# Kernel optimization log

Hardware: AMD Instinct MI355X
Metric: run time of the kernel (lower is better)

The kernel has to match this reference:

```python
import jax, jax.numpy as jnp
import numpy as np

K_NEIGHBORS = 6
LN_EPS = 1e-5


def _layernorm(h, g, b):
    m = h.mean(-1, keepdims=True)
    v = h.var(-1, keepdims=True)
    return (h - m) / jnp.sqrt(v + LN_EPS) * g + b


def _mlp(h, w0, b0, w1, b1):
    return jax.nn.relu(h @ w0 + b0) @ w1 + b1


def _learn_adj(x, Wp, bp):
    # EfficientGraphStructureLearner: cosine-sim topk graph, symmetrized, row-normalized
    h = x @ Wp + bp
    nrm = jnp.linalg.norm(h, axis=1, keepdims=True)
    h = h / jnp.maximum(nrm, 1e-12)
    S = h @ h.T                                  # [N, N]
    vals, idx = jax.lax.top_k(S, K_NEIGHBORS + 1)  # col 0 is self (diag == 1)
    N = x.shape[0]
    rows = jnp.arange(N)[:, None]
    adj = jnp.zeros_like(S).at[rows, idx[:, 1:]].set(vals[:, 1:])
    adj = (adj + adj.T) * 0.5
    adj = adj / (adj.sum(1, keepdims=True) + 1e-8)
    return adj


def _gcn(h, adj, W, b):
    # StandardGraphConv: D^-1/2 (A+I) D^-1/2 @ (h W) + b (diag matmuls as row/col scaling)
    A = adj + jnp.eye(adj.shape[0], dtype=adj.dtype)
    d = jnp.maximum(A.sum(1), 1e-12) ** -0.5
    norm_adj = d[:, None] * A * d[None, :]
    return norm_adj @ (h @ W) + b


def setup_inputs() -> dict:
    key = jax.random.key(0)
    ks = iter(jax.random.split(key, 40))
    N, D, H, O, HP = 8192, 20, 32, 128, 16
    f = lambda *s: jax.random.normal(next(ks), s, dtype=jnp.float32) * 0.1
    inp = {
        'x': jax.random.normal(next(ks), (N, D), dtype=jnp.float32),
        'Wp': f(D, HP), 'bp': jnp.zeros((HP,), jnp.float32),
        'gw0': f(D, H), 'gb0': jnp.zeros((H,), jnp.float32),
        'gw1': f(H, H), 'gb1': jnp.zeros((H,), jnp.float32),
        'gw2': f(H, O), 'gb2': jnp.zeros((O,), jnp.float32),
        'lg0': jnp.ones((H,), jnp.float32), 'lb0': jnp.zeros((H,), jnp.float32),
        'lg1': jnp.ones((H,), jnp.float32), 'lb1': jnp.zeros((H,), jnp.float32),
        'lg2': jnp.ones((O,), jnp.float32), 'lb2': jnp.zeros((O,), jnp.float32),
        'riw0': f(D, H), 'rib0': jnp.zeros((H,), jnp.float32),
        'riw1': f(H, H), 'rib1': jnp.zeros((H,), jnp.float32),
        'rhw0': f(H, H), 'rhb0': jnp.zeros((H,), jnp.float32),
        'rhw1': f(H, H), 'rhb1': jnp.zeros((H,), jnp.float32),
        'row0': f(H, O), 'rob0': jnp.zeros((O,), jnp.float32),
        'row1': f(O, O), 'rob1': jnp.zeros((O,), jnp.float32),
    }
    return inp


def reference(x, Wp, bp, gw0, gb0, gw1, gb1, gw2, gb2,
              lg0, lb0, lg1, lb1, lg2, lb2,
              riw0, rib0, riw1, rib1,
              rhw0, rhb0, rhw1, rhb1,
              row0, rob0, row1, rob1):
    adj = _learn_adj(x, Wp, bp)
    gcns = [(gw0, gb0, lg0, lb0), (gw1, gb1, lg1, lb1), (gw2, gb2, lg2, lb2)]
    skips = [(riw0, rib0, riw1, rib1), (rhw0, rhb0, rhw1, rhb1), (row0, rob0, row1, rob1)]
    h = x
    for i, ((W, b, g, bt), sk) in enumerate(zip(gcns, skips)):
        h_new = jax.nn.relu(_layernorm(_gcn(h, adj, W, b), g, bt))
        h = h_new + _mlp(h, *sk)
        # dropout is identity in eval mode
    return h
```

## Files before the change

### kernel.cpp

```cpp
#include <hip/hip_runtime.h>

constexpr int D_IN = 20;
constexpr int HP   = 16;
constexpr int K    = 6;
constexpr int SAMP = 512;
constexpr int NC   = 8;
constexpr int CAPC = 192;
constexpr int CIN  = 128;
constexpr float MARGIN = 0.02f;

typedef __attribute__((ext_vector_type(8))) short bf16x8;
typedef __attribute__((ext_vector_type(4))) float f32x4;

__device__ __forceinline__ float dot16_seq(const float4* q, const float4* c) {
  float s = 0.f;
#pragma unroll
  for (int m = 0; m < 4; ++m) {
    s = fmaf(q[m].x, c[m].x, s);
    s = fmaf(q[m].y, c[m].y, s);
    s = fmaf(q[m].z, c[m].z, s);
    s = fmaf(q[m].w, c[m].w, s);
  }
  return s;
}

__device__ __forceinline__ short f2bf(float f) {
  unsigned u = __float_as_uint(f);
  unsigned r = (u + 0x7fffu + ((u >> 16) & 1u)) >> 16;
  return (short)r;
}

__device__ __forceinline__ float dinv_of(float own, float ins) {
  float rs = 0.5f * (own + ins);
  float rn = 1.f / (rs + 1e-8f);
  return rsqrtf(fmaxf(1.f + rs * rn, 1e-12f));
}

__global__ void k_proj(const float* __restrict__ x, const float* __restrict__ Wp,
                       const float* __restrict__ bp, const float* __restrict__ gw0,
                       float* __restrict__ hn, short* __restrict__ hnb,
                       float* __restrict__ XW0,
                       float* __restrict__ insum, int* __restrict__ indeg, int N) {
  int i = blockIdx.x * blockDim.x + threadIdx.x;
  if (i >= N) return;
  insum[i] = 0.f; indeg[i] = 0;
  float xr[D_IN];
#pragma unroll
  for (int d = 0; d < D_IN; ++d) xr[d] = x[i*D_IN + d];
  float hv[HP];
  float nrm2 = 0.f;
#pragma unroll
  for (int h = 0; h < HP; ++h) {
    float a = bp[h];
#pragma unroll
    for (int d = 0; d < D_IN; ++d) a += xr[d] * Wp[d*HP + h];
    hv[h] = a;
    nrm2 += a * a;
  }
  float inv = 1.f / fmaxf(sqrtf(nrm2), 1e-12f);
#pragma unroll
  for (int h = 0; h < HP; ++h) {
    float v = hv[h] * inv;
    hn[i*HP + h] = v;
    hnb[(size_t)i*32 + h] = f2bf(v);
  }
#pragma unroll
  for (int h = 0; h < HP; ++h) hnb[(size_t)i*32 + 16 + h] = 0;
#pragma unroll
  for (int oc = 0; oc < 32; ++oc) {
    float a = 0.f;
#pragma unroll
    for (int d = 0; d < D_IN; ++d) a += xr[d] * gw0[d*32 + oc];
    XW0[(size_t)i*32 + oc] = a;
  }
}

struct Top6 { float v0,v1,v2,v3,v4,v5; int i0,i1,i2,i3,i4,i5; };

__device__ __forceinline__ void t6_init(Top6& t) {
  t.v0=t.v1=t.v2=t.v3=t.v4=t.v5=-1e30f;
  t.i0=t.i1=t.i2=t.i3=t.i4=t.i5=-1;
}

#define T6_SWAP(a,b,ia,ib) { float tv=a; a=b; b=tv; int ti=ia; ia=ib; ib=ti; }

__device__ __forceinline__ void t6_insert(Top6& t, float s, int c) {
  if (s > t.v5) {
    t.v5 = s; t.i5 = c;
    if (t.v5 > t.v4) { T6_SWAP(t.v4, t.v5, t.i4, t.i5); }
    if (t.v4 > t.v3) { T6_SWAP(t.v3, t.v4, t.i3, t.i4); }
    if (t.v3 > t.v2) { T6_SWAP(t.v2, t.v3, t.i2, t.i3); }
    if (t.v2 > t.v1) { T6_SWAP(t.v1, t.v2, t.i1, t.i2); }
    if (t.v1 > t.v0) { T6_SWAP(t.v0, t.v1, t.i0, t.i1); }
  }
}

__device__ __forceinline__ void t6_best(const Top6& t, float& cv, int& ci) {
  cv = t.v0; ci = t.i0;
  if (t.v1 > cv || (t.v1 == cv && (unsigned)t.i1 < (unsigned)ci)) { cv = t.v1; ci = t.i1; }
  if (t.v2 > cv || (t.v2 == cv && (unsigned)t.i2 < (unsigned)ci)) { cv = t.v2; ci = t.i2; }
  if (t.v3 > cv || (t.v3 == cv && (unsigned)t.i3 < (unsigned)ci)) { cv = t.v3; ci = t.i3; }
  if (t.v4 > cv || (t.v4 == cv && (unsigned)t.i4 < (unsigned)ci)) { cv = t.v4; ci = t.i4; }
  if (t.v5 > cv || (t.v5 == cv && (unsigned)t.i5 < (unsigned)ci)) { cv = t.v5; ci = t.i5; }
}

__device__ __forceinline__ void t6_consume(Top6& t, int mi) {
  if (t.i0 == mi) t.v0 = -1e30f;
  if (t.i1 == mi) t.v1 = -1e30f;
  if (t.i2 == mi) t.v2 = -1e30f;
  if (t.i3 == mi) t.v3 = -1e30f;
  if (t.i4 == mi) t.v4 = -1e30f;
  if (t.i5 == mi) t.v5 = -1e30f;
}

__global__ __launch_bounds__(256) void k_thresh(const float* __restrict__ hn,
                                                float* __restrict__ tau, int N) {
  int wave = threadIdx.x >> 6, lane = threadIdx.x & 63;
  int row = blockIdx.x * 4 + wave;
  const float4* hn4 = (const float4*)hn;
  float4 q[4];
#pragma unroll
  for (int m = 0; m < 4; ++m) q[m] = hn4[(size_t)row*4 + m];
  Top6 t; t6_init(t);
#pragma unroll
  for (int k = 0; k < SAMP/64; ++k) {
    int c = lane + 64*k;
    if (c != row) {
      float4 cv[4];
#pragma unroll
      for (int m = 0; m < 4; ++m) cv[m] = hn4[(size_t)c*4 + m];
      float s = dot16_seq(q, cv);
      t6_insert(t, s, c);
    }
  }
  float last = -1e30f;
  for (int sel = 0; sel < K; ++sel) {
    float cv; int ci;
    t6_best(t, cv, ci);
    float mv = cv; int mi = ci;
#pragma unroll
    for (int m = 1; m < 64; m <<= 1) {
      float ov = __shfl_xor(mv, m);
      int   oi = __shfl_xor(mi, m);
      if (ov > mv || (ov == mv && (unsigned)oi < (unsigned)mi)) { mv = ov; mi = oi; }
    }
    t6_consume(t, mi);
    last = mv;
  }
  if (lane == 0) tau[row] = last;
}

__global__ __launch_bounds__(256) void k_scan2(
    const short* __restrict__ hnb, const float* __restrict__ tau,
    int* __restrict__ cnt, unsigned short* __restrict__ buf, int N) {
  __shared__ int cntl[16];
  int rb = blockIdx.x / NC;
  int jc = blockIdx.x % NC;
  int wave = threadIdx.x >> 6, lane = threadIdx.x & 63;
  int r0 = rb * 16;
  int half = lane >> 4;
  int l16  = lane & 15;

  if (threadIdx.x < 16) cntl[threadIdx.x] = 0;
  __syncthreads();

  bf16x8 a = *(const bf16x8*)(hnb + (size_t)(r0 + l16)*32 + half*8);
  float4 t4 = *(const float4*)(tau + r0 + half*4);
  float tm0 = t4.x - MARGIN, tm1 = t4.y - MARGIN,
        tm2 = t4.z - MARGIN, tm3 = t4.w - MARGIN;
  f32x4 zero = {0.f, 0.f, 0.f, 0.f};

  const int SPANW = N / NC / 4;
  int jb0 = jc * (N / NC) + wave * SPANW;

#define APPB(R, COND)                                                        \
  {                                                                          \
    unsigned long long mr = __ballot(COND);                                  \
    if (l16 == 0) {                                                          \
      unsigned mask = (unsigned)(mr >> (16*half)) & 0xFFFFu;                 \
      if (mask) {                                                            \
        int row = r0 + half*4 + (R);                                         \
        int pos = atomicAdd(&cntl[4*half + (R)], __popc(mask));              \
        unsigned mm = mask;                                                  \
        while (mm) {                                                         \
          int bx = __ffs(mm) - 1; mm &= mm - 1;                              \
          if (pos < CAPC)                                                    \
            buf[((size_t)row*NC + jc)*CAPC + pos] = (unsigned short)(jb + bx); \
          ++pos;                                                             \
        }                                                                    \
      }                                                                      \
    }                                                                        \
  }

#pragma unroll 4
  for (int jt = 0; jt < SPANW; jt += 16) {
    int jb = jb0 + jt;
    bf16x8 b = *(const bf16x8*)(hnb + (size_t)(jb + l16)*32 + half*8);
    f32x4 d = __builtin_amdgcn_mfma_f32_16x16x32_bf16(a, b, zero, 0, 0, 0);
    bool h0 = d[0] >= tm0, h1 = d[1] >= tm1, h2 = d[2] >= tm2, h3 = d[3] >= tm3;
    if (__any(h0 | h1 | h2 | h3)) {
      APPB(0, h0) APPB(1, h1) APPB(2, h2) APPB(3, h3)
    }
  }
#undef APPB

  __syncthreads();
  if (threadIdx.x < 16)
    cnt[(size_t)(r0 + threadIdx.x)*NC + jc] = min(cntl[threadIdx.x], CAPC);
}

__global__ __launch_bounds__(256) void k_final(
    const float* __restrict__ hn, const unsigned short* __restrict__ buf,
    const int* __restrict__ cnt,
    float* __restrict__ evals, int* __restrict__ eidx,
    float* __restrict__ ownsum, float* insum, int* indeg,
    unsigned short* __restrict__ incol, float* __restrict__ inval, int N) {
  int wave = threadIdx.x >> 6, lane = threadIdx.x & 63;
  int row = blockIdx.x * 4 + wave;
  const float4* hn4 = (const float4*)hn;
  float4 q[4];
#pragma unroll
  for (int m = 0; m < 4; ++m) q[m] = hn4[(size_t)row*4 + m];

  int cbase = row * NC;
  int cl = (lane < NC) ? cnt[cbase + lane] : 0;
  int c0 = __shfl(cl, 0), c1 = __shfl(cl, 1), c2 = __shfl(cl, 2), c3 = __shfl(cl, 3),
      c4 = __shfl(cl, 4), c5 = __shfl(cl, 5), c6 = __shfl(cl, 6), c7 = __shfl(cl, 7);
  int p1 = c0, p2 = p1 + c1, p3 = p2 + c2, p4 = p3 + c3,
      p5 = p4 + c4, p6 = p5 + c5, p7 = p6 + c6, T = p7 + c7;

  Top6 t; t6_init(t);
  for (int e = lane; e < T; e += 64) {
    int s, off;
    if (e < p4) {
      if (e < p2) { if (e < p1) { s = 0; off = e; } else { s = 1; off = e - p1; } }
      else        { if (e < p3) { s = 2; off = e - p2; } else { s = 3; off = e - p3; } }
    } else {
      if (e < p6) { if (e < p5) { s = 4; off = e - p4; } else { s = 5; off = e - p5; } }
      else        { if (e < p7) { s = 6; off = e - p6; } else { s = 7; off = e - p7; } }
    }
    int j = buf[((size_t)cbase + s)*CAPC + off];
    if (j != row) {
      float4 cv[4];
#pragma unroll
      for (int m = 0; m < 4; ++m) cv[m] = hn4[(size_t)j*4 + m];
      float sc = dot16_seq(q, cv);
      t6_insert(t, sc, j);
    }
  }
  float osum = 0.f;
  for (int sel = 0; sel < K; ++sel) {
    float cv; int ci;
    t6_best(t, cv, ci);
    float mv = cv; int mi = ci;
#pragma unroll
    for (int m = 1; m < 64; m <<= 1) {
      float ov = __shfl_xor(mv, m);
      int   oi = __shfl_xor(mi, m);
      if (ov > mv || (ov == mv && (unsigned)oi < (unsigned)mi)) { mv = ov; mi = oi; }
    }
    t6_consume(t, mi);
    if (lane == 0) {
      evals[row*K + sel] = mv;
      eidx [row*K + sel] = mi;
      osum += mv;
      atomicAdd(&insum[mi], mv);
      int pos = atomicAdd(&indeg[mi], 1);
      if (pos < CIN) {
        incol[(size_t)mi*CIN + pos] = (unsigned short)row;
        inval[(size_t)mi*CIN + pos] = mv;
      }
    }
  }
  if (lane == 0) ownsum[row] = osum;
}

template<int DIN, int NEXTD, bool SCALED>
__global__ __launch_bounds__(256) void k_gpost32(
    const float* __restrict__ XWsrc,
    const int* __restrict__ eidx, const float* __restrict__ evals,
    const unsigned short* __restrict__ incol, const float* __restrict__ inval,
    const int* __restrict__ indeg,
    const float* __restrict__ ownsum, const float* __restrict__ insum,
    const float* __restrict__ gb, const float* __restrict__ lg, const float* __restrict__ lb,
    const float* __restrict__ hprev,
    const float* __restrict__ w0, const float* __restrict__ b0,
    const float* __restrict__ w1, const float* __restrict__ b1,
    const float* __restrict__ Wnext, float* __restrict__ XWnext,
    float* __restrict__ outp, int N) {
  __shared__ float hid[4][2][32];
  int tid = threadIdx.x;
  int lane = tid & 63, wslot = tid >> 6;
  int sub = lane >> 5, ol = lane & 31;
  int row = (blockIdx.x * 4 + wslot) * 2 + sub;

  float rs_i = 0.5f * (ownsum[row] + insum[row]);
  float rn_i = 1.f / (rs_i + 1e-8f);
  float di_i = rsqrtf(fmaxf(1.f + rs_i * rn_i, 1e-12f));
  float cc = 0.5f * di_i * rn_i;
  float acc = (SCALED ? di_i : di_i * di_i) * XWsrc[(size_t)row*32 + ol];
#pragma unroll
  for (int t = 0; t < K; ++t) {
    int j = eidx[row*K + t]; float v = evals[row*K + t];
    float cf;
    if constexpr (SCALED) cf = cc * v;
    else                  cf = cc * v * dinv_of(ownsum[j], insum[j]);
    acc = fmaf(cf, XWsrc[(size_t)j*32 + ol], acc);
  }
  int ne = min(indeg[row], CIN);
  for (int e = 0; e < ne; ++e) {
    int j = incol[(size_t)row*CIN + e]; float v = inval[(size_t)row*CIN + e];
    float cf;
    if constexpr (SCALED) cf = cc * v;
    else                  cf = cc * v * dinv_of(ownsum[j], insum[j]);
    acc = fmaf(cf, XWsrc[(size_t)j*32 + ol], acc);
  }
  float u0 = acc + gb[ol];
  float s = u0;
#pragma unroll
  for (int m = 1; m < 32; m <<= 1) s += __shfl_xor(s, m);
  float mean = s * (1.f/32.f);
  float d0 = u0 - mean;
  float vs = d0*d0;
#pragma unroll
  for (int m = 1; m < 32; m <<= 1) vs += __shfl_xor(vs, m);
  float rstd = rsqrtf(vs * (1.f/32.f) + 1e-5f);
  float t0 = fmaxf(d0*rstd*lg[ol] + lb[ol], 0.f);

  float hp[DIN];
#pragma unroll
  for (int d = 0; d < DIN; ++d) hp[d] = hprev[(size_t)row*DIN + d];
  float a = b0[ol];
#pragma unroll
  for (int d = 0; d < DIN; ++d) a = fmaf(hp[d], w0[d*32 + ol], a);
  hid[wslot][sub][ol] = fmaxf(a, 0.f);
  float o = b1[ol];
#pragma unroll
  for (int h = 0; h < 32; ++h) o = fmaf(hid[wslot][sub][h], w1[h*32 + ol], o);
  float hv = t0 + o;
  outp[(size_t)row*32 + ol] = hv;

  hid[wslot][sub][ol] = hv;
#pragma unroll
  for (int k2 = 0; k2 < NEXTD/32; ++k2) {
    int oc = ol + 32*k2;
    float acc2 = 0.f;
#pragma unroll
    for (int d = 0; d < 32; ++d)
      acc2 = fmaf(hid[wslot][sub][d], Wnext[d*NEXTD + oc], acc2);
    XWnext[(size_t)row*NEXTD + oc] = di_i * acc2;
  }
}

__global__ __launch_bounds__(256) void k_gpost128(
    const float* __restrict__ XW,
    const int* __restrict__ eidx, const float* __restrict__ evals,
    const unsigned short* __restrict__ incol, const float* __restrict__ inval,
    const int* __restrict__ indeg,
    const float* __restrict__ ownsum, const float* __restrict__ insum,
    const float* __restrict__ b, const float* __restrict__ g, const float* __restrict__ bt,
    const float* __restrict__ hprev,
    const float* __restrict__ w0, const float* __restrict__ b0,
    const float* __restrict__ w1, const float* __restrict__ b1,
    float* __restrict__ out, int N) {
  __shared__ float hid_s[4][128];
  __shared__ float w1s[2048];
  int wslot = threadIdx.x >> 6;
  int row   = (blockIdx.x * blockDim.x + threadIdx.x) >> 6;
  int lane  = threadIdx.x & 63;
  int o0 = lane, o1 = lane + 64;

  float rs_i = 0.5f * (ownsum[row] + insum[row]);
  float rn_i = 1.f / (rs_i + 1e-8f);
  float di_i = rsqrtf(fmaxf(1.f + rs_i * rn_i, 1e-12f));
  float cc = 0.5f * di_i * rn_i;
  float acc0 = di_i * XW[(size_t)row*128 + o0];
  float acc1 = di_i * XW[(size_t)row*128 + o1];
#pragma unroll
  for (int t = 0; t < K; ++t) {
    int j = eidx[row*K + t];
    float cf = cc * evals[row*K + t];
    acc0 = fmaf(cf, XW[(size_t)j*128 + o0], acc0);
    acc1 = fmaf(cf, XW[(size_t)j*128 + o1], acc1);
  }
  int ne = min(indeg[row], CIN);
  for (int e = 0; e < ne; ++e) {
    int j = incol[(size_t)row*CIN + e];
    float cf = cc * inval[(size_t)row*CIN + e];
    acc0 = fmaf(cf, XW[(size_t)j*128 + o0], acc0);
    acc1 = fmaf(cf, XW[(size_t)j*128 + o1], acc1);
  }
  float u0 = acc0 + b[o0];
  float u1 = acc1 + b[o1];

  float s = u0 + u1;
#pragma unroll
  for (int m = 1; m < 64; m <<= 1) s += __shfl_xor(s, m);
  float mean = s * (1.f/128.f);
  float d0 = u0 - mean, d1 = u1 - mean;
  float vs = d0*d0 + d1*d1;
#pragma unroll
  for (int m = 1; m < 64; m <<= 1) vs += __shfl_xor(vs, m);
  float rstd = rsqrtf(vs * (1.f/128.f) + 1e-5f);
  float t0 = fmaxf(d0*rstd*g[o0] + bt[o0], 0.f);
  float t1 = fmaxf(d1*rstd*g[o1] + bt[o1], 0.f);

  float hp[32];
#pragma unroll
  for (int d = 0; d < 32; ++d) hp[d] = hprev[(size_t)row*32 + d];
  {
    float a = b0[o0];
#pragma unroll
    for (int d = 0; d < 32; ++d) a = fmaf(hp[d], w0[d*128 + o0], a);
    hid_s[wslot][o0] = fmaxf(a, 0.f);
    float a1 = b0[o1];
#pragma unroll
    for (int d = 0; d < 32; ++d) a1 = fmaf(hp[d], w0[d*128 + o1], a1);
    hid_s[wslot][o1] = fmaxf(a1, 0.f);
  }

  float r0=0.f, r1=0.f, r2=0.f, r3=0.f, q0=0.f, q1=0.f, q2=0.f, q3=0.f;
  for (int c = 0; c < 8; ++c) {
    __syncthreads();
    {
      const float4* src = (const float4*)(w1 + c*2048);
      float4* dst = (float4*)w1s;
      dst[threadIdx.x]       = src[threadIdx.x];
      dst[threadIdx.x + 256] = src[threadIdx.x + 256];
    }
    __syncthreads();
    int hb = c*16;
#pragma unroll
    for (int hh = 0; hh < 16; hh += 4) {
      float h0 = hid_s[wslot][hb+hh+0], h1 = hid_s[wslot][hb+hh+1],
            h2 = hid_s[wslot][hb+hh+2], h3 = hid_s[wslot][hb+hh+3];
      r0 = fmaf(h0, w1s[(hh+0)*128 + o0], r0); q0 = fmaf(h0, w1s[(hh+0)*128 + o1], q0);
      r1 = fmaf(h1, w1s[(hh+1)*128 + o0], r1); q1 = fmaf(h1, w1s[(hh+1)*128 + o1], q1);
      r2 = fmaf(h2, w1s[(hh+2)*128 + o0], r2); q2 = fmaf(h2, w1s[(hh+2)*128 + o1], q2);
      r3 = fmaf(h3, w1s[(hh+3)*128 + o0], r3); q3 = fmaf(h3, w1s[(hh+3)*128 + o1], q3);
    }
  }
  out[(size_t)row*128 + o0] = t0 + b1[o0] + ((r0 + r1) + (r2 + r3));
  out[(size_t)row*128 + o1] = t1 + b1[o1] + ((q0 + q1) + (q2 + q3));
}

extern "C" void kernel_launch(void* const* d_in, const int* in_sizes, int n_in,
                              void* d_out, int out_size, void* d_ws, size_t ws_size,
                              hipStream_t stream) {
  const float* x    = (const float*)d_in[0];
  const float* Wp   = (const float*)d_in[1];
  const float* bp   = (const float*)d_in[2];
  const float* gw0  = (const float*)d_in[3];
  const float* gb0  = (const float*)d_in[4];
  const float* gw1  = (const float*)d_in[5];
  const float* gb1  = (const float*)d_in[6];
  const float* gw2  = (const float*)d_in[7];
  const float* gb2  = (const float*)d_in[8];
  const float* lg0  = (const float*)d_in[9];
  const float* lb0  = (const float*)d_in[10];
  const float* lg1  = (const float*)d_in[11];
  const float* lb1  = (const float*)d_in[12];
  const float* lg2  = (const float*)d_in[13];
  const float* lb2  = (const float*)d_in[14];
  const float* riw0 = (const float*)d_in[15];
  const float* rib0 = (const float*)d_in[16];
  const float* riw1 = (const float*)d_in[17];
  const float* rib1 = (const float*)d_in[18];
  const float* rhw0 = (const float*)d_in[19];
  const float* rhb0 = (const float*)d_in[20];
  const float* rhw1 = (const float*)d_in[21];
  const float* rhb1 = (const float*)d_in[22];
  const float* row0 = (const float*)d_in[23];
  const float* rob0 = (const float*)d_in[24];
  const float* row1 = (const float*)d_in[25];
  const float* rob1 = (const float*)d_in[26];
  int N = in_sizes[0] / D_IN;
  float* out = (float*)d_out;

  char* ws = (char*)d_ws;
  size_t off = 0;
  auto alloc = [&](size_t bytes) -> void* {
    void* p = ws + off;
    off += (bytes + 255) & ~(size_t)255;
    return p;
  };
  float* hn      = (float*)alloc((size_t)N * HP * 4);
  float* evals   = (float*)alloc((size_t)N * K * 4);
  int*   eidx    = (int*)  alloc((size_t)N * K * 4);
  float* ownsum  = (float*)alloc((size_t)N * 4);
  float* insum   = (float*)alloc((size_t)N * 4);
  int*   indeg   = (int*)  alloc((size_t)N * 4);
  float* XWa     = (float*)alloc((size_t)N * 128 * 4);
  float* XWb     = (float*)alloc((size_t)N * 32 * 4);
  float* h1      = (float*)alloc((size_t)N * 32 * 4);
  float* h2      = (float*)alloc((size_t)N * 32 * 4);
  float* tau     = (float*)alloc((size_t)N * 4);
  int*   cnt     = (int*)  alloc((size_t)N * NC * 4);
  unsigned short* buf = (unsigned short*)alloc((size_t)N * NC * CAPC * 2);
  short* hnb     = (short*)alloc((size_t)N * 32 * 2);
  unsigned short* incol = (unsigned short*)alloc((size_t)N * CIN * 2);
  float* inval   = (float*)alloc((size_t)N * CIN * 4);
  (void)ws_size; (void)n_in; (void)out_size;

  const int B = 256;
  hipLaunchKernelGGL(k_proj, dim3((N + B - 1) / B), dim3(B), 0, stream,
                     x, Wp, bp, gw0, hn, hnb, XWa, insum, indeg, N);
  hipLaunchKernelGGL(k_thresh, dim3(N / 4), dim3(B), 0, stream, hn, tau, N);
  hipLaunchKernelGGL(k_scan2, dim3((N / 16) * NC), dim3(B), 0, stream, hnb, tau, cnt, buf, N);
  hipLaunchKernelGGL(k_final, dim3(N / 4), dim3(B), 0, stream,
                     hn, buf, cnt, evals, eidx, ownsum, insum, indeg, incol, inval, N);

  hipLaunchKernelGGL((k_gpost32<20, 32, false>), dim3(N / 8), dim3(B), 0, stream,
                     XWa, eidx, evals, incol, inval, indeg, ownsum, insum,
                     gb0, lg0, lb0, x, riw0, rib0, riw1, rib1, gw1, XWb, h1, N);
  hipLaunchKernelGGL((k_gpost32<32, 128, true>), dim3(N / 8), dim3(B), 0, stream,
                     XWb, eidx, evals, incol, inval, indeg, ownsum, insum,
                     gb1, lg1, lb1, h1, rhw0, rhb0, rhw1, rhb1, gw2, XWa, h2, N);
  hipLaunchKernelGGL(k_gpost128, dim3(N / 4), dim3(B), 0, stream,
                     XWa, eidx, evals, incol, inval, indeg, ownsum, insum,
                     gb2, lg2, lb2, h2, row0, rob0, row1, rob1, out, N);
}
```

Before: 151.5 us.

## Fuse threshold, MFMA scan and final top-k into one block-per-16-rows kernel

Merges the sampled-threshold, MFMA candidate-scan and final exact top-k kernels into a single 1024-thread kernel that handles 16 rows per block. Thresholds and candidate lists stay in LDS instead of going through global tau/cnt/buf arrays, which removes two launches and the global scatter/gather of candidates. The trade-off is that each block now scans all N columns for its 16 rows with 16 waves, where before the column range was split across 8 blocks, so there is less grid parallelism (512 blocks) and heavier LDS atomics. The hprev load loop split is a no-op.

```diff
diff --git a/kernel.cpp b/kernel.cpp
--- a/kernel.cpp
+++ b/kernel.cpp
@@ -4,8 +4,7 @@
 constexpr int HP   = 16;
 constexpr int K    = 6;
 constexpr int SAMP = 512;
-constexpr int NC   = 8;
-constexpr int CAPC = 192;
+constexpr int CAPL = 384;
 constexpr int CIN  = 128;
 constexpr float MARGIN = 0.02f;
 
@@ -113,166 +112,141 @@
   if (t.i5 == mi) t.v5 = -1e30f;
 }
 
-__global__ __launch_bounds__(256) void k_thresh(const float* __restrict__ hn,
-                                                float* __restrict__ tau, int N) {
-  int wave = threadIdx.x >> 6, lane = threadIdx.x & 63;
-  int row = blockIdx.x * 4 + wave;
-  const float4* hn4 = (const float4*)hn;
-  float4 q[4];
-#pragma unroll
-  for (int m = 0; m < 4; ++m) q[m] = hn4[(size_t)row*4 + m];
-  Top6 t; t6_init(t);
-#pragma unroll
-  for (int k = 0; k < SAMP/64; ++k) {
-    int c = lane + 64*k;
-    if (c != row) {
-      float4 cv[4];
-#pragma unroll
-      for (int m = 0; m < 4; ++m) cv[m] = hn4[(size_t)c*4 + m];
-      float s = dot16_seq(q, cv);
-      t6_insert(t, s, c);
-    }
-  }
-  float last = -1e30f;
-  for (int sel = 0; sel < K; ++sel) {
-    float cv; int ci;
-    t6_best(t, cv, ci);
-    float mv = cv; int mi = ci;
-#pragma unroll
-    for (int m = 1; m < 64; m <<= 1) {
-      float ov = __shfl_xor(mv, m);
-      int   oi = __shfl_xor(mi, m);
-      if (ov > mv || (ov == mv && (unsigned)oi < (unsigned)mi)) { mv = ov; mi = oi; }
-    }
-    t6_consume(t, mi);
-    last = mv;
-  }
-  if (lane == 0) tau[row] = last;
-}
-
-__global__ __launch_bounds__(256) void k_scan2(
-    const short* __restrict__ hnb, const float* __restrict__ tau,
-    int* __restrict__ cnt, unsigned short* __restrict__ buf, int N) {
-  __shared__ int cntl[16];
-  int rb = blockIdx.x / NC;
-  int jc = blockIdx.x % NC;
-  int wave = threadIdx.x >> 6, lane = threadIdx.x & 63;
-  int r0 = rb * 16;
-  int half = lane >> 4;
-  int l16  = lane & 15;
-
-  if (threadIdx.x < 16) cntl[threadIdx.x] = 0;
-  __syncthreads();
-
-  bf16x8 a = *(const bf16x8*)(hnb + (size_t)(r0 + l16)*32 + half*8);
-  float4 t4 = *(const float4*)(tau + r0 + half*4);
-  float tm0 = t4.x - MARGIN, tm1 = t4.y - MARGIN,
-        tm2 = t4.z - MARGIN, tm3 = t4.w - MARGIN;
-  f32x4 zero = {0.f, 0.f, 0.f, 0.f};
-
-  const int SPANW = N / NC / 4;
-  int jb0 = jc * (N / NC) + wave * SPANW;
-
-#define APPB(R, COND)                                                        \
-  {                                                                          \
-    unsigned long long mr = __ballot(COND);                                  \
-    if (l16 == 0) {                                                          \
-      unsigned mask = (unsigned)(mr >> (16*half)) & 0xFFFFu;                 \
-      if (mask) {                                                            \
-        int row = r0 + half*4 + (R);                                         \
-        int pos = atomicAdd(&cntl[4*half + (R)], __popc(mask));              \
-        unsigned mm = mask;                                                  \
-        while (mm) {                                                         \
-          int bx = __ffs(mm) - 1; mm &= mm - 1;                              \
-          if (pos < CAPC)                                                    \
-            buf[((size_t)row*NC + jc)*CAPC + pos] = (unsigned short)(jb + bx); \
-          ++pos;                                                             \
-        }                                                                    \
-      }                                                                      \
-    }                                                                        \
-  }
-
-#pragma unroll 4
-  for (int jt = 0; jt < SPANW; jt += 16) {
-    int jb = jb0 + jt;
-    bf16x8 b = *(const bf16x8*)(hnb + (size_t)(jb + l16)*32 + half*8);
-    f32x4 d = __builtin_amdgcn_mfma_f32_16x16x32_bf16(a, b, zero, 0, 0, 0);
-    bool h0 = d[0] >= tm0, h1 = d[1] >= tm1, h2 = d[2] >= tm2, h3 = d[3] >= tm3;
-    if (__any(h0 | h1 | h2 | h3)) {
-      APPB(0, h0) APPB(1, h1) APPB(2, h2) APPB(3, h3)
-    }
-  }
-#undef APPB
-
-  __syncthreads();
-  if (threadIdx.x < 16)
-    cnt[(size_t)(r0 + threadIdx.x)*NC + jc] = min(cntl[threadIdx.x], CAPC);
-}
-
-__global__ __launch_bounds__(256) void k_final(
-    const float* __restrict__ hn, const unsigned short* __restrict__ buf,
-    const int* __restrict__ cnt,
+__global__ __launch_bounds__(1024) void k_scanfin(
+    const float* __restrict__ hn, const short* __restrict__ hnb,
     float* __restrict__ evals, int* __restrict__ eidx,
     float* __restrict__ ownsum, float* insum, int* indeg,
     unsigned short* __restrict__ incol, float* __restrict__ inval, int N) {
-  int wave = threadIdx.x >> 6, lane = threadIdx.x & 63;
-  int row = blockIdx.x * 4 + wave;
+  __shared__ unsigned short hbuf[16][CAPL];
+  __shared__ int cntl[16];
+  __shared__ float tau_s[16];
+  int tid = threadIdx.x;
+  int wave = tid >> 6, lane = tid & 63;
+  int r0 = blockIdx.x * 16;
   const float4* hn4 = (const float4*)hn;
-  float4 q[4];
-#pragma unroll
-  for (int m = 0; m < 4; ++m) q[m] = hn4[(size_t)row*4 + m];
-
-  int cbase = row * NC;
-  int cl = (lane < NC) ? cnt[cbase + lane] : 0;
-  int c0 = __shfl(cl, 0), c1 = __shfl(cl, 1), c2 = __shfl(cl, 2), c3 = __shfl(cl, 3),
-      c4 = __shfl(cl, 4), c5 = __shfl(cl, 5), c6 = __shfl(cl, 6), c7 = __shfl(cl, 7);
-  int p1 = c0, p2 = p1 + c1, p3 = p2 + c2, p4 = p3 + c3,
-      p5 = p4 + c4, p6 = p5 + c5, p7 = p6 + c6, T = p7 + c7;
-
-  Top6 t; t6_init(t);
-  for (int e = lane; e < T; e += 64) {
-    int s, off;
-    if (e < p4) {
-      if (e < p2) { if (e < p1) { s = 0; off = e; } else { s = 1; off = e - p1; } }
-      else        { if (e < p3) { s = 2; off = e - p2; } else { s = 3; off = e - p3; } }
-    } else {
-      if (e < p6) { if (e < p5) { s = 4; off = e - p4; } else { s = 5; off = e - p5; } }
-      else        { if (e < p7) { s = 6; off = e - p6; } else { s = 7; off = e - p7; } }
-    }
-    int j = buf[((size_t)cbase + s)*CAPC + off];
-    if (j != row) {
-      float4 cv[4];
-#pragma unroll
-      for (int m = 0; m < 4; ++m) cv[m] = hn4[(size_t)j*4 + m];
-      float sc = dot16_seq(q, cv);
-      t6_insert(t, sc, j);
-    }
-  }
-  float osum = 0.f;
-  for (int sel = 0; sel < K; ++sel) {
-    float cv; int ci;
-    t6_best(t, cv, ci);
-    float mv = cv; int mi = ci;
-#pragma unroll
-    for (int m = 1; m < 64; m <<= 1) {
-      float ov = __shfl_xor(mv, m);
-      int   oi = __shfl_xor(mi, m);
-      if (ov > mv || (ov == mv && (unsigned)oi < (unsigned)mi)) { mv = ov; mi = oi; }
-    }
-    t6_consume(t, mi);
-    if (lane == 0) {
-      evals[row*K + sel] = mv;
-      eidx [row*K + sel] = mi;
-      osum += mv;
-      atomicAdd(&insum[mi], mv);
-      int pos = atomicAdd(&indeg[mi], 1);
-      if (pos < CIN) {
-        incol[(size_t)mi*CIN + pos] = (unsigned short)row;
-        inval[(size_t)mi*CIN + pos] = mv;
-      }
-    }
-  }
-  if (lane == 0) ownsum[row] = osum;
+
+  if (tid < 16) cntl[tid] = 0;
+
+  {
+    int row = r0 + wave;
+    float4 q[4];
+#pragma unroll
+    for (int m = 0; m < 4; ++m) q[m] = hn4[(size_t)row*4 + m];
+    Top6 t; t6_init(t);
+#pragma unroll
+    for (int k = 0; k < SAMP/64; ++k) {
+      int c = lane + 64*k;
+      if (c != row) {
+        float4 cv[4];
+#pragma unroll
+        for (int m = 0; m < 4; ++m) cv[m] = hn4[(size_t)c*4 + m];
+        float s = dot16_seq(q, cv);
+        t6_insert(t, s, c);
+      }
+    }
+    float last = -1e30f;
+    for (int sel = 0; sel < K; ++sel) {
+      float cv; int ci;
+      t6_best(t, cv, ci);
+      float mv = cv; int mi = ci;
+#pragma unroll
+      for (int m = 1; m < 64; m <<= 1) {
+        float ov = __shfl_xor(mv, m);
+        int   oi = __shfl_xor(mi, m);
+        if (ov > mv || (ov == mv && (unsigned)oi < (unsigned)mi)) { mv = ov; mi = oi; }
+      }
+      t6_consume(t, mi);
+      last = mv;
+    }
+    if (lane == 0) tau_s[wave] = last;
+  }
+  __syncthreads();
+
+  {
+    int half = lane >> 4;
+    int l16  = lane & 15;
+    bf16x8 a = *(const bf16x8*)(hnb + (size_t)(r0 + l16)*32 + half*8);
+    float tm0 = tau_s[half*4+0] - MARGIN, tm1 = tau_s[half*4+1] - MARGIN,
+          tm2 = tau_s[half*4+2] - MARGIN, tm3 = tau_s[half*4+3] - MARGIN;
+    f32x4 zero = {0.f, 0.f, 0.f, 0.f};
+    const int SPANW = N / 16;
+    int jb0 = wave * SPANW;
+
+#define APPB(R, COND)                                                        \
+    {                                                                        \
+      unsigned long long mr = __ballot(COND);                                \
+      if (l16 == 0) {                                                        \
+        unsigned mask = (unsigned)(mr >> (16*half)) & 0xFFFFu;               \
+        if (mask) {                                                          \
+          int rl = 4*half + (R);                                             \
+          int pos = atomicAdd(&cntl[rl], __popc(mask));                      \
+          unsigned mm = mask;                                                \
+          while (mm) {                                                       \
+            int bx = __ffs(mm) - 1; mm &= mm - 1;                            \
+            if (pos < CAPL) hbuf[rl][pos] = (unsigned short)(jb + bx);       \
+            ++pos;                                                           \
+          }                                                                  \
+        }                                                                    \
+      }                                                                      \
+    }
+
+#pragma unroll 4
+    for (int jt = 0; jt < SPANW; jt += 16) {
+      int jb = jb0 + jt;
+      bf16x8 b = *(const bf16x8*)(hnb + (size_t)(jb + l16)*32 + half*8);
+      f32x4 d = __builtin_amdgcn_mfma_f32_16x16x32_bf16(a, b, zero, 0, 0, 0);
+      bool h0 = d[0] >= tm0, h1 = d[1] >= tm1, h2 = d[2] >= tm2, h3 = d[3] >= tm3;
+      if (__any(h0 | h1 | h2 | h3)) {
+        APPB(0, h0) APPB(1, h1) APPB(2, h2) APPB(3, h3)
+      }
+    }
+#undef APPB
+  }
+  __syncthreads();
+
+  {
+    int row = r0 + wave;
+    int n = min(cntl[wave], CAPL);
+    float4 q[4];
+#pragma unroll
+    for (int m = 0; m < 4; ++m) q[m] = hn4[(size_t)row*4 + m];
+    Top6 t; t6_init(t);
+    for (int e = lane; e < n; e += 64) {
+      int j = hbuf[wave][e];
+      if (j != row) {
+        float4 cv[4];
+#pragma unroll
+        for (int m = 0; m < 4; ++m) cv[m] = hn4[(size_t)j*4 + m];
+        float sc = dot16_seq(q, cv);
+        t6_insert(t, sc, j);
+      }
+    }
+    float osum = 0.f;
+    for (int sel = 0; sel < K; ++sel) {
+      float cv; int ci;
+      t6_best(t, cv, ci);
+      float mv = cv; int mi = ci;
+#pragma unroll
+      for (int m = 1; m < 64; m <<= 1) {
+        float ov = __shfl_xor(mv, m);
+        int   oi = __shfl_xor(mi, m);
+        if (ov > mv || (ov == mv && (unsigned)oi < (unsigned)mi)) { mv = ov; mi = oi; }
+      }
+      t6_consume(t, mi);
+      if (lane == 0) {
+        evals[row*K + sel] = mv;
+        eidx [row*K + sel] = mi;
+        osum += mv;
+        atomicAdd(&insum[mi], mv);
+        int pos = atomicAdd(&indeg[mi], 1);
+        if (pos < CIN) {
+          incol[(size_t)mi*CIN + pos] = (unsigned short)row;
+          inval[(size_t)mi*CIN + pos] = mv;
+        }
+      }
+    }
+    if (lane == 0) ownsum[row] = osum;
+  }
 }
 
 template<int DIN, int NEXTD, bool SCALED>
@@ -329,7 +303,9 @@
 
   float hp[DIN];
 #pragma unroll
-  for (int d = 0; d < DIN; ++d) hp[d] = hprev[(size_t)row*DIN + d];
+  for (int d = 0; d < D_IN && d < DIN; ++d) hp[d] = hprev[(size_t)row*DIN + d];
+#pragma unroll
+  for (int d = (D_IN < DIN ? D_IN : DIN); d < DIN; ++d) hp[d] = hprev[(size_t)row*DIN + d];
   float a = b0[ol];
 #pragma unroll
   for (int d = 0; d < DIN; ++d) a = fmaf(hp[d], w0[d*32 + ol], a);
@@ -494,9 +470,6 @@
   float* XWb     = (float*)alloc((size_t)N * 32 * 4);
   float* h1      = (float*)alloc((size_t)N * 32 * 4);
   float* h2      = (float*)alloc((size_t)N * 32 * 4);
-  float* tau     = (float*)alloc((size_t)N * 4);
-  int*   cnt     = (int*)  alloc((size_t)N * NC * 4);
-  unsigned short* buf = (unsigned short*)alloc((size_t)N * NC * CAPC * 2);
   short* hnb     = (short*)alloc((size_t)N * 32 * 2);
   unsigned short* incol = (unsigned short*)alloc((size_t)N * CIN * 2);
   float* inval   = (float*)alloc((size_t)N * CIN * 4);
@@ -505,10 +478,8 @@
   const int B = 256;
   hipLaunchKernelGGL(k_proj, dim3((N + B - 1) / B), dim3(B), 0, stream,
                      x, Wp, bp, gw0, hn, hnb, XWa, insum, indeg, N);
-  hipLaunchKernelGGL(k_thresh, dim3(N / 4), dim3(B), 0, stream, hn, tau, N);
-  hipLaunchKernelGGL(k_scan2, dim3((N / 16) * NC), dim3(B), 0, stream, hnb, tau, cnt, buf, N);
-  hipLaunchKernelGGL(k_final, dim3(N / 4), dim3(B), 0, stream,
-                     hn, buf, cnt, evals, eidx, ownsum, insum, indeg, incol, inval, N);
+  hipLaunchKernelGGL(k_scanfin, dim3(N / 16), dim3(1024), 0, stream,
+                     hn, hnb, evals, eidx, ownsum, insum, indeg, incol, inval, N);
 
   hipLaunchKernelGGL((k_gpost32<20, 32, false>), dim3(N / 8), dim3(B), 0, stream,
                      XWa, eidx, evals, incol, inval, indeg, ownsum, insum,
```

After: 147.8 us. 1.03x faster.
